# Kernel tuning notes

Measured on AMD Instinct MI355X. Metric: run time of the kernel, lower is better.

## Reference

```python
import jax, jax.numpy as jnp
import numpy as np

TEMP = 0.05


def setup_inputs() -> dict:
    key = jax.random.key(0)
    k1, k2, k3 = jax.random.split(key, 3)
    B, D, NC = 1024, 256, 50000  # batch, feat dim, num clusters
    inputs = jax.random.normal(k1, (B, D), dtype=jnp.float32)
    targets = jax.random.randint(k2, (B,), 0, NC, dtype=jnp.int64)
    feats = jax.random.normal(k3, (2 * NC, D), dtype=jnp.float32)
    # memory bank rows are kept L2-normalized by the module's update rule
    feats = feats / jnp.linalg.norm(feats, axis=1, keepdims=True)
    return {"inputs": inputs, "targets": targets, "features": feats}


def reference(inputs, targets, features):
    # F.normalize(inputs, dim=1)
    x = inputs / jnp.linalg.norm(inputs, axis=1, keepdims=True)
    # outputs = x @ features.T / temp  -> [B, 2*NC]
    logits = jnp.matmul(x, features.T) / TEMP
    mean_logits, hard_logits = jnp.split(logits, 2, axis=1)  # each [B, NC]

    def ce(lg):
        logp = jax.nn.log_softmax(lg, axis=1)
        return -jnp.take_along_axis(logp, targets[:, None], axis=1).mean()

    loss = 0.5 * (ce(hard_logits) + ce(mean_logits))
    return loss
```

## Files before the change

### kernel.cpp

```cpp
#include <hip/hip_runtime.h>
#include <math.h>

#define BATCH 1024
#define DIM   256
#define NCL   50000
#define TOTC  100000
#define NSLICE 16

typedef __attribute__((ext_vector_type(8)))  short bf16x8;
typedef __attribute__((ext_vector_type(16))) float f32x16;

__device__ __forceinline__ unsigned short f2bf(float f) {
    unsigned int u = __float_as_uint(f);
    return (unsigned short)((u + 0x7FFFu + ((u >> 16) & 1u)) >> 16);
}

__global__ __launch_bounds__(64) void k_prep(const float* __restrict__ in,
                                             const int* __restrict__ tgt,
                                             const float* __restrict__ feats,
                                             unsigned short* __restrict__ xnT,
                                             float* __restrict__ Sx,
                                             float* __restrict__ z) {
    const int b = blockIdx.x;
    const int t = threadIdx.x;
    float4 v = *(const float4*)&in[b * DIM + t * 4];
    float ss = v.x * v.x + v.y * v.y + v.z * v.z + v.w * v.w;
#pragma unroll
    for (int o = 1; o < 64; o <<= 1) ss += __shfl_xor(ss, o, 64);
    const float sc = 1.0f / sqrtf(ss);
    float4 w;
    w.x = v.x * sc; w.y = v.y * sc; w.z = v.z * sc; w.w = v.w * sc;

    uint2 p;
    p.x = (unsigned int)f2bf(w.x) | ((unsigned int)f2bf(w.y) << 16);
    p.y = (unsigned int)f2bf(w.z) | ((unsigned int)f2bf(w.w) << 16);
    *(uint2*)((char*)xnT + (t >> 1) * 16384 + b * 16 + (t & 1) * 8) = p;

    const int tb = tgt[b];
#pragma unroll
    for (int h = 0; h < 2; ++h) {
        const int row = tb + h * NCL;
        float4 f = *(const float4*)&feats[row * DIM + t * 4];
        float d = w.x * f.x + w.y * f.y + w.z * f.z + w.w * f.w;
#pragma unroll
        for (int o = 1; o < 64; o <<= 1) d += __shfl_xor(d, o, 64);
        if (t == 0) z[b * 2 + h] = d * 20.0f;
    }
    if (t < 32) Sx[b * 32 + t] = 0.0f;
}

__global__ __launch_bounds__(512) void k_main(const unsigned short* __restrict__ xnT,
                                              const float* __restrict__ feats,
                                              float* __restrict__ Sx) {
    __shared__ unsigned short Ab[128 * 256];

    const int tid  = threadIdx.x;
    const int lane = tid & 63;
    const int wid  = tid >> 6;
    const int wm   = wid >> 2;
    const int wn   = wid & 3;
    const int l31  = lane & 31;
    const int hi   = lane >> 5;
    const int cb0  = blockIdx.x * 128;
    float* Ss = Sx + (blockIdx.x & (NSLICE - 1)) * (BATCH * 2);

#pragma unroll
    for (int it = 0; it < 16; ++it) {
        const int f  = it * 512 + tid;
        const int r  = f >> 6;
        const int c4 = f & 63;
        int gr = cb0 + r;
        if (gr > TOTC - 1) gr = TOTC - 1;
        const float4 v = *(const float4*)&feats[(size_t)gr * DIM + c4 * 4];
        uint2 p;
        p.x = (unsigned int)f2bf(v.x) | ((unsigned int)f2bf(v.y) << 16);
        p.y = (unsigned int)f2bf(v.z) | ((unsigned int)f2bf(v.w) << 16);
        const int byte = r * 512 + (((c4 >> 1) * 16) ^ ((r & 7) << 4)) + (c4 & 1) * 8;
        *(uint2*)((char*)Ab + byte) = p;
    }
    __syncthreads();

    const bool mixed = (cb0 < NCL && cb0 + 127 >= NCL) || (cb0 + 127 >= TOTC);
    const int  halfsel = (cb0 >= NCL) ? 1 : 0;

    const int r0 = wm * 64 + l31;
    const int r1 = r0 + 32;
    const int swz = (r0 & 7) << 4;

    float sreg0[8], sreg1[8];

#pragma unroll
    for (int bt = 0; bt < 8; ++bt) {
        const unsigned short* bb = xnT + (size_t)hi * (BATCH * 8)
                                 + (size_t)(bt * 128 + wn * 32 + l31) * 8;

        f32x16 acc0 = (f32x16)(0.0f), acc1 = (f32x16)(0.0f);
#pragma unroll
        for (int kk = 0; kk < 16; ++kk) {
            const bf16x8 bf = *(const bf16x8*)(bb + (size_t)kk * 16384);
            const int kb = ((kk * 2 + hi) * 16) ^ swz;
            const bf16x8 a0 = *(const bf16x8*)((const char*)Ab + r0 * 512 + kb);
            const bf16x8 a1 = *(const bf16x8*)((const char*)Ab + r1 * 512 + kb);
            acc0 = __builtin_amdgcn_mfma_f32_32x32x16_bf16(a0, bf, acc0, 0, 0, 0);
            acc1 = __builtin_amdgcn_mfma_f32_32x32x16_bf16(a1, bf, acc1, 0, 0, 0);
        }

        if (!mixed) {
            float s = 0.0f;
#pragma unroll
            for (int r = 0; r < 16; ++r) {
                s += __expf(fmaf(acc0[r], 20.0f, -20.0f));
                s += __expf(fmaf(acc1[r], 20.0f, -20.0f));
            }
            s += __shfl_xor(s, 32, 64);
            sreg0[bt] = s;
            sreg1[bt] = 0.0f;
        } else {
            float sh0 = 0.0f, sh1 = 0.0f;
#pragma unroll
            for (int mt = 0; mt < 2; ++mt)
#pragma unroll
                for (int r = 0; r < 16; ++r) {
                    const int cl = cb0 + wm * 64 + mt * 32 +
                                   (r & 3) + 8 * (r >> 2) + 4 * hi;
                    const bool valid = cl < TOTC;
                    float e = __expf(fmaf((mt ? acc1[r] : acc0[r]), 20.0f, -20.0f));
                    e = valid ? e : 0.0f;
                    sh0 += (cl < NCL) ? e : 0.0f;
                    sh1 += (cl < NCL) ? 0.0f : e;
                }
            sh0 += __shfl_xor(sh0, 32, 64);
            sh1 += __shfl_xor(sh1, 32, 64);
            sreg0[bt] = sh0;
            sreg1[bt] = sh1;
        }
    }

    if (hi == 0) {
        if (!mixed) {
#pragma unroll
            for (int bt = 0; bt < 8; ++bt) {
                const int bcol = bt * 128 + wn * 32 + l31;
                atomicAdd(&Ss[bcol * 2 + halfsel], sreg0[bt]);
            }
        } else {
#pragma unroll
            for (int bt = 0; bt < 8; ++bt) {
                const int bcol = bt * 128 + wn * 32 + l31;
                atomicAdd(&Ss[bcol * 2 + 0], sreg0[bt]);
                atomicAdd(&Ss[bcol * 2 + 1], sreg1[bt]);
            }
        }
    }
}

__global__ __launch_bounds__(256) void k_loss(const float* __restrict__ Sx,
                                              const float* __restrict__ z,
                                              float* __restrict__ out) {
    const int t = threadIdx.x;
    float part = 0.0f;
    for (int r = t; r < BATCH; r += 256) {
        float s0 = 0.0f, s1 = 0.0f;
#pragma unroll
        for (int sl = 0; sl < NSLICE; ++sl) {
            s0 += Sx[sl * (BATCH * 2) + r * 2 + 0];
            s1 += Sx[sl * (BATCH * 2) + r * 2 + 1];
        }
        part += 40.0f + logf(s0) + logf(s1) - z[r * 2 + 0] - z[r * 2 + 1];
    }
#pragma unroll
    for (int o = 1; o < 64; o <<= 1) part += __shfl_xor(part, o, 64);
    __shared__ float ws[4];
    if ((t & 63) == 0) ws[t >> 6] = part;
    __syncthreads();
    if (t == 0) {
        const float tot = ws[0] + ws[1] + ws[2] + ws[3];
        out[0] = 0.5f * tot / (float)BATCH;
    }
}

extern "C" void kernel_launch(void* const* d_in, const int* in_sizes, int n_in,
                              void* d_out, int out_size, void* d_ws, size_t ws_size,
                              hipStream_t stream) {
    const float* inputs  = (const float*)d_in[0];
    const int*   targets = (const int*)d_in[1];
    const float* feats   = (const float*)d_in[2];
    float* out = (float*)d_out;

    unsigned short* xnT = (unsigned short*)d_ws;
    float* Sx = (float*)(xnT + BATCH * DIM);
    float* zt = Sx + NSLICE * BATCH * 2;

    k_prep<<<BATCH, 64, 0, stream>>>(inputs, targets, feats, xnT, Sx, zt);
    const int nblk = (TOTC + 127) / 128;
    k_main<<<nblk, 512, 0, stream>>>(xnT, feats, Sx);
    k_loss<<<1, 256, 0, stream>>>(Sx, zt, out);
}
```

Before: 92.15 us.

## Retile main GEMM so each wave covers all 128 clusters and 64 batch columns

```diff
diff --git a/kernel.cpp b/kernel.cpp
--- a/kernel.cpp
+++ b/kernel.cpp
@@ -10,9 +10,9 @@
 typedef __attribute__((ext_vector_type(8)))  short bf16x8;
 typedef __attribute__((ext_vector_type(16))) float f32x16;
 
-__device__ __forceinline__ unsigned short f2bf(float f) {
+__device__ __forceinline__ unsigned int f2bf(float f) {
     unsigned int u = __float_as_uint(f);
-    return (unsigned short)((u + 0x7FFFu + ((u >> 16) & 1u)) >> 16);
+    return (u + 0x7FFFu + ((u >> 16) & 1u)) >> 16;
 }
 
 __global__ __launch_bounds__(64) void k_prep(const float* __restrict__ in,
@@ -32,8 +32,8 @@
     w.x = v.x * sc; w.y = v.y * sc; w.z = v.z * sc; w.w = v.w * sc;
 
     uint2 p;
-    p.x = (unsigned int)f2bf(w.x) | ((unsigned int)f2bf(w.y) << 16);
-    p.y = (unsigned int)f2bf(w.z) | ((unsigned int)f2bf(w.w) << 16);
+    p.x = f2bf(w.x) | (f2bf(w.y) << 16);
+    p.y = f2bf(w.z) | (f2bf(w.w) << 16);
     *(uint2*)((char*)xnT + (t >> 1) * 16384 + b * 16 + (t & 1) * 8) = p;
 
     const int tb = tgt[b];
@@ -56,101 +56,114 @@
 
     const int tid  = threadIdx.x;
     const int lane = tid & 63;
-    const int wid  = tid >> 6;
-    const int wm   = wid >> 2;
-    const int wn   = wid & 3;
+    const int wn   = tid >> 6;
     const int l31  = lane & 31;
     const int hi   = lane >> 5;
     const int cb0  = blockIdx.x * 128;
     float* Ss = Sx + (blockIdx.x & (NSLICE - 1)) * (BATCH * 2);
 
 #pragma unroll
-    for (int it = 0; it < 16; ++it) {
-        const int f  = it * 512 + tid;
-        const int r  = f >> 6;
-        const int c4 = f & 63;
+    for (int it = 0; it < 8; ++it) {
+        const int idx = it * 512 + tid;
+        const int r = idx >> 5;
+        const int c = idx & 31;
         int gr = cb0 + r;
         if (gr > TOTC - 1) gr = TOTC - 1;
-        const float4 v = *(const float4*)&feats[(size_t)gr * DIM + c4 * 4];
-        uint2 p;
-        p.x = (unsigned int)f2bf(v.x) | ((unsigned int)f2bf(v.y) << 16);
-        p.y = (unsigned int)f2bf(v.z) | ((unsigned int)f2bf(v.w) << 16);
-        const int byte = r * 512 + (((c4 >> 1) * 16) ^ ((r & 7) << 4)) + (c4 & 1) * 8;
-        *(uint2*)((char*)Ab + byte) = p;
+        const float4 f0 = *(const float4*)&feats[(size_t)gr * DIM + c * 8];
+        const float4 f1 = *(const float4*)&feats[(size_t)gr * DIM + c * 8 + 4];
+        uint4 pk;
+        pk.x = f2bf(f0.x) | (f2bf(f0.y) << 16);
+        pk.y = f2bf(f0.z) | (f2bf(f0.w) << 16);
+        pk.z = f2bf(f1.x) | (f2bf(f1.y) << 16);
+        pk.w = f2bf(f1.z) | (f2bf(f1.w) << 16);
+        *(uint4*)((char*)Ab + c * 2048 + ((r * 16) ^ ((c & 7) << 4))) = pk;
     }
     __syncthreads();
 
     const bool mixed = (cb0 < NCL && cb0 + 127 >= NCL) || (cb0 + 127 >= TOTC);
     const int  halfsel = (cb0 >= NCL) ? 1 : 0;
 
-    const int r0 = wm * 64 + l31;
-    const int r1 = r0 + 32;
-    const int swz = (r0 & 7) << 4;
-
-    float sreg0[8], sreg1[8];
-
-#pragma unroll
-    for (int bt = 0; bt < 8; ++bt) {
-        const unsigned short* bb = xnT + (size_t)hi * (BATCH * 8)
-                                 + (size_t)(bt * 128 + wn * 32 + l31) * 8;
-
-        f32x16 acc0 = (f32x16)(0.0f), acc1 = (f32x16)(0.0f);
-#pragma unroll
+    float sr0[2][2], sr1[2][2];
+
+#pragma unroll
+    for (int p = 0; p < 2; ++p) {
+        const unsigned short* bb0 = xnT + (size_t)hi * 8192
+                                  + (size_t)(p * 512 + wn * 64 + l31) * 8;
+        const unsigned short* bb1 = bb0 + 256;
+
+        f32x16 acc[4][2];
+#pragma unroll
+        for (int mt = 0; mt < 4; ++mt) {
+            acc[mt][0] = (f32x16)(0.0f);
+            acc[mt][1] = (f32x16)(0.0f);
+        }
+
+#pragma unroll 4
         for (int kk = 0; kk < 16; ++kk) {
-            const bf16x8 bf = *(const bf16x8*)(bb + (size_t)kk * 16384);
-            const int kb = ((kk * 2 + hi) * 16) ^ swz;
-            const bf16x8 a0 = *(const bf16x8*)((const char*)Ab + r0 * 512 + kb);
-            const bf16x8 a1 = *(const bf16x8*)((const char*)Ab + r1 * 512 + kb);
-            acc0 = __builtin_amdgcn_mfma_f32_32x32x16_bf16(a0, bf, acc0, 0, 0, 0);
-            acc1 = __builtin_amdgcn_mfma_f32_32x32x16_bf16(a1, bf, acc1, 0, 0, 0);
+            const bf16x8 b0 = *(const bf16x8*)(bb0 + (size_t)kk * 16384);
+            const bf16x8 b1 = *(const bf16x8*)(bb1 + (size_t)kk * 16384);
+            const int ch = kk * 2 + hi;
+            const int kbase = ch * 2048;
+            const int key = (ch & 7) << 4;
+#pragma unroll
+            for (int mt = 0; mt < 4; ++mt) {
+                const bf16x8 a = *(const bf16x8*)((const char*)Ab + kbase
+                                   + ((mt * 512 + l31 * 16) ^ key));
+                acc[mt][0] = __builtin_amdgcn_mfma_f32_32x32x16_bf16(a, b0, acc[mt][0], 0, 0, 0);
+                acc[mt][1] = __builtin_amdgcn_mfma_f32_32x32x16_bf16(a, b1, acc[mt][1], 0, 0, 0);
+            }
         }
 
         if (!mixed) {
-            float s = 0.0f;
-#pragma unroll
-            for (int r = 0; r < 16; ++r) {
-                s += __expf(fmaf(acc0[r], 20.0f, -20.0f));
-                s += __expf(fmaf(acc1[r], 20.0f, -20.0f));
-            }
-            s += __shfl_xor(s, 32, 64);
-            sreg0[bt] = s;
-            sreg1[bt] = 0.0f;
+#pragma unroll
+            for (int nn = 0; nn < 2; ++nn) {
+                float s = 0.0f;
+#pragma unroll
+                for (int mt = 0; mt < 4; ++mt)
+#pragma unroll
+                    for (int r = 0; r < 16; ++r)
+                        s += __expf(fmaf(acc[mt][nn][r], 20.0f, -20.0f));
+                s += __shfl_xor(s, 32, 64);
+                sr0[p][nn] = s;
+                sr1[p][nn] = 0.0f;
+            }
         } else {
-            float sh0 = 0.0f, sh1 = 0.0f;
-#pragma unroll
-            for (int mt = 0; mt < 2; ++mt)
-#pragma unroll
-                for (int r = 0; r < 16; ++r) {
-                    const int cl = cb0 + wm * 64 + mt * 32 +
-                                   (r & 3) + 8 * (r >> 2) + 4 * hi;
-                    const bool valid = cl < TOTC;
-                    float e = __expf(fmaf((mt ? acc1[r] : acc0[r]), 20.0f, -20.0f));
-                    e = valid ? e : 0.0f;
-                    sh0 += (cl < NCL) ? e : 0.0f;
-                    sh1 += (cl < NCL) ? 0.0f : e;
+#pragma unroll
+            for (int nn = 0; nn < 2; ++nn) {
+                float sh0 = 0.0f, sh1 = 0.0f;
+#pragma unroll
+                for (int mt = 0; mt < 4; ++mt)
+#pragma unroll
+                    for (int r = 0; r < 16; ++r) {
+                        const int cl = cb0 + mt * 32 +
+                                       (r & 3) + 8 * (r >> 2) + 4 * hi;
+                        const bool valid = cl < TOTC;
+                        float e = __expf(fmaf(acc[mt][nn][r], 20.0f, -20.0f));
+                        e = valid ? e : 0.0f;
+                        sh0 += (cl < NCL) ? e : 0.0f;
+                        sh1 += (cl < NCL) ? 0.0f : e;
+                    }
+                sh0 += __shfl_xor(sh0, 32, 64);
+                sh1 += __shfl_xor(sh1, 32, 64);
+                sr0[p][nn] = sh0;
+                sr1[p][nn] = sh1;
+            }
+        }
+    }
+
+    if (hi == 0) {
+#pragma unroll
+        for (int p = 0; p < 2; ++p)
+#pragma unroll
+            for (int nn = 0; nn < 2; ++nn) {
+                const int col = p * 512 + wn * 64 + nn * 32 + l31;
+                if (!mixed) {
+                    atomicAdd(&Ss[col * 2 + halfsel], sr0[p][nn]);
+                } else {
+                    atomicAdd(&Ss[col * 2 + 0], sr0[p][nn]);
+                    atomicAdd(&Ss[col * 2 + 1], sr1[p][nn]);
                 }
-            sh0 += __shfl_xor(sh0, 32, 64);
-            sh1 += __shfl_xor(sh1, 32, 64);
-            sreg0[bt] = sh0;
-            sreg1[bt] = sh1;
-        }
-    }
-
-    if (hi == 0) {
-        if (!mixed) {
-#pragma unroll
-            for (int bt = 0; bt < 8; ++bt) {
-                const int bcol = bt * 128 + wn * 32 + l31;
-                atomicAdd(&Ss[bcol * 2 + halfsel], sreg0[bt]);
-            }
-        } else {
-#pragma unroll
-            for (int bt = 0; bt < 8; ++bt) {
-                const int bcol = bt * 128 + wn * 32 + l31;
-                atomicAdd(&Ss[bcol * 2 + 0], sreg0[bt]);
-                atomicAdd(&Ss[bcol * 2 + 1], sreg1[bt]);
-            }
-        }
+            }
     }
 }
 
```

After: 98.74 us. +7.2%, slower.
